# Kernel tuning notes

Hardware: AMD Instinct MI355X
Metric: run time of the kernel (lower is better)

## Reference

```python
import jax, jax.numpy as jnp
import numpy as np

TEMP = 0.05
EPS = 1e-8  # F.cosine_similarity eps

def setup_inputs() -> dict:
    key = jax.random.key(0)
    k1, k2 = jax.random.split(key)
    cls = jax.random.normal(k1, (4096, 1024), dtype=jnp.float32)
    hidden = jax.random.normal(k2, (4096, 1024), dtype=jnp.float32)
    return {"cls": cls, "hidden": hidden}

def _normalize(x):
    # matches F.cosine_similarity: divide by max(||x||, eps)
    n = jnp.sqrt(jnp.sum(x * x, axis=-1, keepdims=True))
    return x / jnp.maximum(n, EPS)

def reference(cls, hidden):
    a = _normalize(cls)          # [B, H]
    b = _normalize(hidden)       # [B, H]
    sim = jnp.einsum('ih,jh->ij', a, b) / TEMP  # [B, B] cosine sims / temp
    # cross-entropy with labels = arange(B): mean(logsumexp(row) - diag)
    lse = jax.nn.logsumexp(sim, axis=-1)        # [B]
    diag = jnp.diagonal(sim)                    # [B]
    return jnp.mean(lse - diag)
```

## Files before the change

kernel.cpp:

```cpp
#include <hip/hip_runtime.h>
#include <hip/hip_bf16.h>

typedef __attribute__((ext_vector_type(8))) short bf16x8;
typedef __attribute__((ext_vector_type(4))) float f32x4;

#define B_ROWS 4096
#define H_DIM  1024
#define TEMP_INV 20.0f
#define BM 256
#define BK 32
#define NT (H_DIM / BK)
#define NBN (B_ROWS / BM)

__device__ __forceinline__ void gload_lds16(const void* g, void* l) {
  __builtin_amdgcn_global_load_lds(
      (const __attribute__((address_space(1))) void*)g,
      (__attribute__((address_space(3))) void*)l, 16, 0, 0);
}

__global__ __launch_bounds__(256) void normalize_kernel(
    const float* __restrict__ cls, const float* __restrict__ hid,
    __hip_bfloat16* __restrict__ Abf, __hip_bfloat16* __restrict__ Bbf,
    float* __restrict__ out)
{
  if (blockIdx.x == 0 && threadIdx.x == 0) out[0] = 0.0f;
  const int w = threadIdx.x >> 6, lane = threadIdx.x & 63;
  const int r = blockIdx.x * 4 + w;
  const int rr = r & (B_ROWS - 1);
  const float* src = ((r < B_ROWS) ? cls : hid) + (size_t)rr * H_DIM;
  __hip_bfloat16* dst = ((r < B_ROWS) ? Abf : Bbf) + (size_t)rr * H_DIM;

  float4 v[4];
  float ss = 0.f;
  #pragma unroll
  for (int j = 0; j < 4; j++) {
    v[j] = reinterpret_cast<const float4*>(src)[j * 64 + lane];
    ss += v[j].x * v[j].x + v[j].y * v[j].y + v[j].z * v[j].z + v[j].w * v[j].w;
  }
  #pragma unroll
  for (int off = 1; off < 64; off <<= 1) ss += __shfl_xor(ss, off, 64);
  const float scale = 1.0f / fmaxf(sqrtf(ss), 1e-8f);

  #pragma unroll
  for (int j = 0; j < 4; j++) {
    union { ushort4 u; __hip_bfloat16 h[4]; } o;
    o.h[0] = __float2bfloat16(v[j].x * scale);
    o.h[1] = __float2bfloat16(v[j].y * scale);
    o.h[2] = __float2bfloat16(v[j].z * scale);
    o.h[3] = __float2bfloat16(v[j].w * scale);
    reinterpret_cast<ushort4*>(dst)[j * 64 + lane] = o.u;
  }
}


#define STAGE4(BUF, TT)                                                       \
  { gload_lds16(Abase + (size_t)(row0 + 0   + srow) * 2048 + (TT) * 64 + scolb, \
                &As[BUF][tid * 16]);                                          \
    gload_lds16(Abase + (size_t)(row0 + 128 + srow) * 2048 + (TT) * 64 + scolb, \
                &As[BUF][8192 + tid * 16]);                                   \
    gload_lds16(Bbase + (size_t)(col0 + 0   + srow) * 2048 + (TT) * 64 + scolb, \
                &Bs[BUF][tid * 16]);                                          \
    gload_lds16(Bbase + (size_t)(col0 + 128 + srow) * 2048 + (TT) * 64 + scolb, \
                &Bs[BUF][8192 + tid * 16]); }

#define RDFRAGS(BC)                                                           \
  { _Pragma("unroll") for (int mi = 0; mi < 8; mi++)                          \
      af[mi] = *(const bf16x8*)(&As[BC][rA + mi * 1024]);                     \
    _Pragma("unroll") for (int ni = 0; ni < 4; ni++)                          \
      bfr[ni] = *(const bf16x8*)(&Bs[BC][rB + ni * 1024]); }

#define MFMA32()                                                              \
  { __builtin_amdgcn_s_setprio(1);                                            \
    _Pragma("unroll") for (int mi = 0; mi < 8; mi++) {                        \
      _Pragma("unroll") for (int ni = 0; ni < 4; ni++) {                      \
        acc[mi][ni] = __builtin_amdgcn_mfma_f32_16x16x32_bf16(                \
            af[mi], bfr[ni], acc[mi][ni], 0, 0, 0); } }                       \
    __builtin_amdgcn_s_setprio(0); }

#define BARB() __builtin_amdgcn_s_barrier()

#define ITER_F(T_, BC)                                                        \
  { STAGE4((BC + 3) & 3, (T_) + 3); RDFRAGS(BC); MFMA32();                    \
    asm volatile("s_waitcnt vmcnt(8)" ::: "memory"); BARB(); }

__global__ __launch_bounds__(512, 2) void gemm_kernel(
    const __hip_bfloat16* __restrict__ A, const __hip_bfloat16* __restrict__ Bm,
    float* __restrict__ pp, float* __restrict__ diag)
{
  __shared__ __align__(16) char As[4][16384];
  __shared__ __align__(16) char Bs[4][16384];

  const int tid  = threadIdx.x;
  const int lane = tid & 63;
  const int w    = tid >> 6;
  const int wm   = w >> 2, wn = w & 3;

  const int fid = blockIdx.y * NBN + blockIdx.x;
  const int swz = (fid & 7) * 32 + (fid >> 3);
  const int bm = swz >> 4, bn = swz & 15;

  const long row0 = (long)bm * BM, col0 = (long)bn * BM;
  const char* Abase = (const char*)A;
  const char* Bbase = (const char*)Bm;

  const int srow  = tid >> 2;
  const int scolb = (((tid & 3) ^ ((tid >> 3) & 3)) << 4);

  const int fr  = lane & 15;
  const int xsl = ((lane >> 4) * 16) ^ ((fr & 6) << 3);
  const int rA  = (wm * 128 + fr) * 64 + xsl;
  const int rB  = (wn * 64  + fr) * 64 + xsl;

  f32x4 acc[8][4] = {};
  bf16x8 af[8], bfr[4];

  STAGE4(0, 0);
  STAGE4(1, 1);
  STAGE4(2, 2);
  asm volatile("s_waitcnt vmcnt(8)" ::: "memory");
  BARB();

  #pragma unroll 1
  for (int T = 0; T < 28; T += 4) {
    ITER_F(T,     0);
    ITER_F(T + 1, 1);
    ITER_F(T + 2, 2);
    ITER_F(T + 3, 3);
  }
  { STAGE4(3, 31); RDFRAGS(0); MFMA32();
    asm volatile("s_waitcnt vmcnt(8)" ::: "memory"); BARB(); }
  { RDFRAGS(1); MFMA32();
    asm volatile("s_waitcnt vmcnt(4)" ::: "memory"); BARB(); }
  { RDFRAGS(2); MFMA32();
    asm volatile("s_waitcnt vmcnt(0)" ::: "memory"); BARB(); }
  { RDFRAGS(3); MFMA32(); }

  const bool isdiag = (bm == bn);
  const int g = lane >> 4;
  __syncthreads();
  float* lds_p = (float*)&As[0][0];

  #pragma unroll
  for (int m = 0; m < 8; m++) {
    const int rowb = (int)row0 + wm * 128 + m * 16 + g * 4;
    float p[4] = {0.f, 0.f, 0.f, 0.f};
    #pragma unroll
    for (int n = 0; n < 4; n++) {
      const int colb = (int)col0 + wn * 64 + n * 16 + fr;
      #pragma unroll
      for (int r = 0; r < 4; r++) {
        float sim = acc[m][n][r] * TEMP_INV;
        if (isdiag && (rowb + r == colb)) diag[rowb + r] = sim;
        p[r] += __expf(sim);
      }
    }
    #pragma unroll
    for (int r = 0; r < 4; r++) {
      float s = p[r];
      s += __shfl_xor(s, 1, 64);
      s += __shfl_xor(s, 2, 64);
      s += __shfl_xor(s, 4, 64);
      s += __shfl_xor(s, 8, 64);
      if (fr == 0)
        lds_p[wn * 256 + wm * 128 + m * 16 + g * 4 + r] = s;
    }
  }
  __syncthreads();
  if (tid < 256) {
    float s = lds_p[tid] + lds_p[256 + tid] + lds_p[512 + tid] + lds_p[768 + tid];
    pp[(size_t)bn * B_ROWS + row0 + tid] = s;
  }
}

__global__ __launch_bounds__(256) void finalize_kernel(
    const float* __restrict__ pp, const float* __restrict__ diag,
    float* __restrict__ out)
{
  const int tid = threadIdx.x;
  const int i = blockIdx.x * 256 + tid;
  float s = 0.f;
  #pragma unroll
  for (int j = 0; j < NBN; j++) s += pp[(size_t)j * B_ROWS + i];
  float acc = logf(s) - diag[i];
  #pragma unroll
  for (int off = 1; off < 64; off <<= 1) acc += __shfl_xor(acc, off, 64);
  __shared__ float wsum[4];
  if ((tid & 63) == 0) wsum[tid >> 6] = acc;
  __syncthreads();
  if (tid == 0) {
    float t = wsum[0] + wsum[1] + wsum[2] + wsum[3];
    atomicAdd(out, t * (1.0f / B_ROWS));
  }
}

extern "C" void kernel_launch(void* const* d_in, const int* in_sizes, int n_in,
                              void* d_out, int out_size, void* d_ws, size_t ws_size,
                              hipStream_t stream)
{
  const float* cls = (const float*)d_in[0];
  const float* hid = (const float*)d_in[1];
  float* out = (float*)d_out;
  char* ws = (char*)d_ws;

  __hip_bfloat16* Abf = (__hip_bfloat16*)ws;
  __hip_bfloat16* Bbf = (__hip_bfloat16*)(ws + (size_t)B_ROWS * H_DIM * 2);
  float* pp   = (float*)(ws + (size_t)B_ROWS * H_DIM * 4);
  float* diag = pp + (size_t)NBN * B_ROWS;

  hipLaunchKernelGGL(normalize_kernel, dim3(2 * B_ROWS / 4), dim3(256), 0, stream,
                     cls, hid, Abf, Bbf, out);
  hipLaunchKernelGGL(gemm_kernel, dim3(NBN, NBN), dim3(512), 0, stream,
                     Abf, Bbf, pp, diag);
  hipLaunchKernelGGL(finalize_kernel, dim3(B_ROWS / 256), dim3(256), 0, stream,
                     pp, diag, out);
}
```

Baseline: 113.3 us.

## Quantize normalized inputs to FP8 and use scaled 16x16x128 MFMA

The normalize kernel now writes FP8 (e4m3) instead of bf16. The GEMM uses the MX-scaled f8f6f4 MFMA with unit scales, K-tile 128 and a two-stage double buffer. This halves operand bandwidth and doubles MFMA throughput per instruction. The cost is precision: temperature 0.05 amplifies FP8 rounding error in the logits. The pipeline also becomes shallower (wait for all loads, then a barrier each step), and an unused COMPUTE macro is left behind.

```diff
diff --git a/kernel.cpp b/kernel.cpp
--- a/kernel.cpp
+++ b/kernel.cpp
@@ -1,14 +1,15 @@
 #include <hip/hip_runtime.h>
 #include <hip/hip_bf16.h>
 
-typedef __attribute__((ext_vector_type(8))) short bf16x8;
+typedef __attribute__((ext_vector_type(4))) int   i32x4;
+typedef __attribute__((ext_vector_type(8))) int   i32x8;
 typedef __attribute__((ext_vector_type(4))) float f32x4;
 
 #define B_ROWS 4096
 #define H_DIM  1024
 #define TEMP_INV 20.0f
 #define BM 256
-#define BK 32
+#define BK 128
 #define NT (H_DIM / BK)
 #define NBN (B_ROWS / BM)
 
@@ -20,7 +21,7 @@
 
 __global__ __launch_bounds__(256) void normalize_kernel(
     const float* __restrict__ cls, const float* __restrict__ hid,
-    __hip_bfloat16* __restrict__ Abf, __hip_bfloat16* __restrict__ Bbf,
+    unsigned char* __restrict__ Aq, unsigned char* __restrict__ Bq,
     float* __restrict__ out)
 {
   if (blockIdx.x == 0 && threadIdx.x == 0) out[0] = 0.0f;
@@ -28,7 +29,7 @@
   const int r = blockIdx.x * 4 + w;
   const int rr = r & (B_ROWS - 1);
   const float* src = ((r < B_ROWS) ? cls : hid) + (size_t)rr * H_DIM;
-  __hip_bfloat16* dst = ((r < B_ROWS) ? Abf : Bbf) + (size_t)rr * H_DIM;
+  unsigned char* dst = ((r < B_ROWS) ? Aq : Bq) + (size_t)rr * H_DIM;
 
   float4 v[4];
   float ss = 0.f;
@@ -43,52 +44,44 @@
 
   #pragma unroll
   for (int j = 0; j < 4; j++) {
-    union { ushort4 u; __hip_bfloat16 h[4]; } o;
-    o.h[0] = __float2bfloat16(v[j].x * scale);
-    o.h[1] = __float2bfloat16(v[j].y * scale);
-    o.h[2] = __float2bfloat16(v[j].z * scale);
-    o.h[3] = __float2bfloat16(v[j].w * scale);
-    reinterpret_cast<ushort4*>(dst)[j * 64 + lane] = o.u;
-  }
-}
-
-
-#define STAGE4(BUF, TT)                                                       \
-  { gload_lds16(Abase + (size_t)(row0 + 0   + srow) * 2048 + (TT) * 64 + scolb, \
-                &As[BUF][tid * 16]);                                          \
-    gload_lds16(Abase + (size_t)(row0 + 128 + srow) * 2048 + (TT) * 64 + scolb, \
-                &As[BUF][8192 + tid * 16]);                                   \
-    gload_lds16(Bbase + (size_t)(col0 + 0   + srow) * 2048 + (TT) * 64 + scolb, \
-                &Bs[BUF][tid * 16]);                                          \
-    gload_lds16(Bbase + (size_t)(col0 + 128 + srow) * 2048 + (TT) * 64 + scolb, \
-                &Bs[BUF][8192 + tid * 16]); }
-
-#define RDFRAGS(BC)                                                           \
-  { _Pragma("unroll") for (int mi = 0; mi < 8; mi++)                          \
-      af[mi] = *(const bf16x8*)(&As[BC][rA + mi * 1024]);                     \
+    int p = __builtin_amdgcn_cvt_pk_fp8_f32(v[j].x * scale, v[j].y * scale, 0, false);
+    p = __builtin_amdgcn_cvt_pk_fp8_f32(v[j].z * scale, v[j].w * scale, p, true);
+    reinterpret_cast<int*>(dst)[j * 64 + lane] = p;
+  }
+}
+
+
+#define BARB() __builtin_amdgcn_s_barrier()
+
+#define STAGE_A(BUF, TT, C)                                                   \
+  gload_lds16(Abase + (size_t)(row0 + (C) * 64 + srow) * 1024 + (TT) * 128 + scolb, \
+              &As[BUF][(C) * 8192 + tid * 16])
+#define STAGE_B(BUF, TT, C)                                                   \
+  gload_lds16(Bbase + (size_t)(col0 + (C) * 64 + srow) * 1024 + (TT) * 128 + scolb, \
+              &Bs[BUF][(C) * 8192 + tid * 16])
+
+#define STAGE8(BUF, TT)                                                       \
+  { STAGE_A(BUF, TT, 0); STAGE_A(BUF, TT, 1); STAGE_A(BUF, TT, 2);            \
+    STAGE_A(BUF, TT, 3); STAGE_B(BUF, TT, 0); STAGE_B(BUF, TT, 1);            \
+    STAGE_B(BUF, TT, 2); STAGE_B(BUF, TT, 3); }
+
+#define RD8(ARR, OFF, DST)                                                    \
+  { i32x4 lo_ = *(const i32x4*)(&ARR[(OFF)]);                                 \
+    i32x4 hi_ = *(const i32x4*)(&ARR[(OFF) ^ 16]);                            \
+    DST = __builtin_shufflevector(lo_, hi_, 0, 1, 2, 3, 4, 5, 6, 7); }
+
+#define COMPUTE(BUF)                                                          \
+  { i32x8 bfr[4];                                                             \
     _Pragma("unroll") for (int ni = 0; ni < 4; ni++)                          \
-      bfr[ni] = *(const bf16x8*)(&Bs[BC][rB + ni * 1024]); }
-
-#define MFMA32()                                                              \
-  { __builtin_amdgcn_s_setprio(1);                                            \
-    _Pragma("unroll") for (int mi = 0; mi < 8; mi++) {                        \
-      _Pragma("unroll") for (int ni = 0; ni < 4; ni++) {                      \
-        acc[mi][ni] = __builtin_amdgcn_mfma_f32_16x16x32_bf16(                \
-            af[mi], bfr[ni], acc[mi][ni], 0, 0, 0); } }                       \
-    __builtin_amdgcn_s_setprio(0); }
-
-#define BARB() __builtin_amdgcn_s_barrier()
-
-#define ITER_F(T_, BC)                                                        \
-  { STAGE4((BC + 3) & 3, (T_) + 3); RDFRAGS(BC); MFMA32();                    \
-    asm volatile("s_waitcnt vmcnt(8)" ::: "memory"); BARB(); }
+      RD8(As , 0, bfr[ni]);                                          \
+  }
 
 __global__ __launch_bounds__(512, 2) void gemm_kernel(
-    const __hip_bfloat16* __restrict__ A, const __hip_bfloat16* __restrict__ Bm,
+    const unsigned char* __restrict__ A, const unsigned char* __restrict__ Bm,
     float* __restrict__ pp, float* __restrict__ diag)
 {
-  __shared__ __align__(16) char As[4][16384];
-  __shared__ __align__(16) char Bs[4][16384];
+  __shared__ __align__(16) char As[2][32768];
+  __shared__ __align__(16) char Bs[2][32768];
 
   const int tid  = threadIdx.x;
   const int lane = tid & 63;
@@ -103,37 +96,44 @@
   const char* Abase = (const char*)A;
   const char* Bbase = (const char*)Bm;
 
-  const int srow  = tid >> 2;
-  const int scolb = (((tid & 3) ^ ((tid >> 3) & 3)) << 4);
-
-  const int fr  = lane & 15;
-  const int xsl = ((lane >> 4) * 16) ^ ((fr & 6) << 3);
-  const int rA  = (wm * 128 + fr) * 64 + xsl;
-  const int rB  = (wn * 64  + fr) * 64 + xsl;
+  const int srow  = tid >> 3;
+  const int scolb = (((tid & 7) ^ ((tid >> 3) & 7)) << 4);
+
+  const int fr = lane & 15;
+  const int rA = (wm * 128 + fr) * 128 + (((lane >> 4) * 2 ^ (fr & 7)) << 4);
+  const int rB = (wn * 64  + fr) * 128 + (((lane >> 4) * 2 ^ (fr & 7)) << 4);
 
   f32x4 acc[8][4] = {};
-  bf16x8 af[8], bfr[4];
-
-  STAGE4(0, 0);
-  STAGE4(1, 1);
-  STAGE4(2, 2);
-  asm volatile("s_waitcnt vmcnt(8)" ::: "memory");
+
+  STAGE8(0, 0);
+  asm volatile("s_waitcnt vmcnt(0)" ::: "memory");
   BARB();
 
-  #pragma unroll 1
-  for (int T = 0; T < 28; T += 4) {
-    ITER_F(T,     0);
-    ITER_F(T + 1, 1);
-    ITER_F(T + 2, 2);
-    ITER_F(T + 3, 3);
-  }
-  { STAGE4(3, 31); RDFRAGS(0); MFMA32();
-    asm volatile("s_waitcnt vmcnt(8)" ::: "memory"); BARB(); }
-  { RDFRAGS(1); MFMA32();
-    asm volatile("s_waitcnt vmcnt(4)" ::: "memory"); BARB(); }
-  { RDFRAGS(2); MFMA32();
-    asm volatile("s_waitcnt vmcnt(0)" ::: "memory"); BARB(); }
-  { RDFRAGS(3); MFMA32(); }
+  #pragma unroll
+  for (int T = 0; T < NT; T++) {
+    if (T + 1 < NT) STAGE8((T + 1) & 1, T + 1);
+    const int BUF = T & 1;
+    i32x8 bfr[4];
+    #pragma unroll
+    for (int ni = 0; ni < 4; ni++)
+      RD8(Bs[BUF], rB + ni * 2048, bfr[ni]);
+    #pragma unroll
+    for (int mi = 0; mi < 8; mi++) {
+      i32x8 afm;
+      RD8(As[BUF], rA + mi * 2048, afm);
+      __builtin_amdgcn_s_setprio(1);
+      #pragma unroll
+      for (int ni = 0; ni < 4; ni++)
+        acc[mi][ni] = __builtin_amdgcn_mfma_scale_f32_16x16x128_f8f6f4(
+            afm, bfr[ni], acc[mi][ni], 0, 0,
+            0, 0x7F7F7F7F, 0, 0x7F7F7F7F);
+      __builtin_amdgcn_s_setprio(0);
+    }
+    if (T + 1 < NT) {
+      asm volatile("s_waitcnt vmcnt(0)" ::: "memory");
+      BARB();
+    }
+  }
 
   const bool isdiag = (bm == bn);
   const int g = lane >> 4;
@@ -202,15 +202,15 @@
   float* out = (float*)d_out;
   char* ws = (char*)d_ws;
 
-  __hip_bfloat16* Abf = (__hip_bfloat16*)ws;
-  __hip_bfloat16* Bbf = (__hip_bfloat16*)(ws + (size_t)B_ROWS * H_DIM * 2);
-  float* pp   = (float*)(ws + (size_t)B_ROWS * H_DIM * 4);
+  unsigned char* Aq = (unsigned char*)ws;
+  unsigned char* Bq = (unsigned char*)(ws + (size_t)B_ROWS * H_DIM);
+  float* pp   = (float*)(ws + (size_t)B_ROWS * H_DIM * 2);
   float* diag = pp + (size_t)NBN * B_ROWS;
 
   hipLaunchKernelGGL(normalize_kernel, dim3(2 * B_ROWS / 4), dim3(256), 0, stream,
-                     cls, hid, Abf, Bbf, out);
+                     cls, hid, Aq, Bq, out);
   hipLaunchKernelGGL(gemm_kernel, dim3(NBN, NBN), dim3(512), 0, stream,
-                     Abf, Bbf, pp, diag);
+                     Aq, Bq, pp, diag);
   hipLaunchKernelGGL(finalize_kernel, dim3(B_ROWS / 256), dim3(256), 0, stream,
                      pp, diag, out);
 }
```

Measured after the change: 277.9 us. 2.45x slower.
